# Kernel optimization log

Measured on AMD Instinct MI355X. Metric: run time of the kernel, lower is better.

## Reference

```python
import jax, jax.numpy as jnp
import numpy as np


def setup_inputs() -> dict:
    key = jax.random.key(0)
    ks = jax.random.split(key, 10)
    B, T, E = 4096, 200, 64
    H0, H1, H2 = 80, 40, 1
    D = 4 * E  # concat feature dim = 256
    glorot = lambda k, shp: jax.random.normal(k, shp, jnp.float32) * jnp.sqrt(2.0 / (shp[0] + shp[1]))
    return {
        "queries": jax.random.normal(ks[0], (B, 1, E), jnp.float32),
        "keys": jax.random.normal(ks[1], (B, T, E), jnp.float32),
        "keys_length": jax.random.randint(ks[2], (B, 1), 0, T, jnp.int32),
        "W0": glorot(ks[3], (D, H0)),
        "b0": jnp.zeros((H0,), jnp.float32),
        "W1": glorot(ks[4], (H0, H1)),
        "b1": jnp.zeros((H1,), jnp.float32),
        "W2": glorot(ks[5], (H1, H2)),
        "b2": jnp.zeros((H2,), jnp.float32),
    }


def reference(queries, keys, keys_length, W0, b0, W1, b1, W2, b2):
    B, T, E = keys.shape
    # repeat query along history axis: [B,1,E] -> [B,T,E]
    q = jnp.broadcast_to(queries, (B, T, E))
    # DIN attention input: [B,T,4E]
    att = jnp.concatenate([q, keys, q - keys, q * keys], axis=-1)
    # tiny 3-layer MLP, sigmoid activations (att_activation, no output_activation override)
    h = jax.nn.sigmoid(att @ W0 + b0)
    h = jax.nn.sigmoid(h @ W1 + b1)
    score = jax.nn.sigmoid(h @ W2 + b2)          # [B,T,1]
    out = jnp.transpose(score, (0, 2, 1))         # [B,1,T]
    # sequence mask: [B,1,T]
    key_masks = jnp.arange(T)[None, None, :] < keys_length[:, :, None]
    # weight_normalization=False -> masked positions become 0, no softmax
    out = jnp.where(key_masks, out, jnp.zeros_like(out))
    # weighted sum over history: [B,1,T] @ [B,T,E] -> [B,1,E]
    return jnp.matmul(out, keys)
```

## Files before the change

kernel.cpp:

```cpp
#include <hip/hip_runtime.h>

#define NT 512
#define NWAVE 8
#define PE 136
#define PW1 104
#define PH 104

typedef __attribute__((ext_vector_type(8))) short short8;
typedef __attribute__((ext_vector_type(4))) float f32x4;

#define DPP_ADD(x, ctrl)                                                    \
  ((x) + __uint_as_float(__builtin_amdgcn_mov_dpp(                          \
             __float_as_uint(x), (ctrl), 0xf, 0xf, true)))

__device__ __forceinline__ unsigned short f2b(float f) {
  unsigned int x = __float_as_uint(f);
  return (unsigned short)((x + 0x7fffu + ((x >> 16) & 1u)) >> 16);
}
__device__ __forceinline__ float b2f(unsigned short u) {
  return __uint_as_float(((unsigned int)u) << 16);
}
__device__ __forceinline__ float sigmoidf(float x) {
  return __builtin_amdgcn_rcpf(1.0f + __expf(-x));
}
__device__ __forceinline__ short8 pack8(float4 a, float4 b) {
  short8 r;
  r[0] = (short)f2b(a.x); r[1] = (short)f2b(a.y); r[2] = (short)f2b(a.z); r[3] = (short)f2b(a.w);
  r[4] = (short)f2b(b.x); r[5] = (short)f2b(b.y); r[6] = (short)f2b(b.z); r[7] = (short)f2b(b.w);
  return r;
}
__device__ __forceinline__ short8 pack8qb(float4 a, float4 b, short8 qp) {
  short8 r;
  r[0] = (short)f2b(a.x * b2f((unsigned short)qp[0]));
  r[1] = (short)f2b(a.y * b2f((unsigned short)qp[1]));
  r[2] = (short)f2b(a.z * b2f((unsigned short)qp[2]));
  r[3] = (short)f2b(a.w * b2f((unsigned short)qp[3]));
  r[4] = (short)f2b(b.x * b2f((unsigned short)qp[4]));
  r[5] = (short)f2b(b.y * b2f((unsigned short)qp[5]));
  r[6] = (short)f2b(b.z * b2f((unsigned short)qp[6]));
  r[7] = (short)f2b(b.w * b2f((unsigned short)qp[7]));
  return r;
}

__global__ __launch_bounds__(256, 2) void prep_c(
    const float* __restrict__ q, const float* __restrict__ W0,
    const float* __restrict__ b0, float* __restrict__ C, int B)
{
  __shared__ float Wac[64 * 80];
  __shared__ float qlds[32 * 64];
  const int bbase = blockIdx.x * 32, tid = threadIdx.x;
  for (int idx = tid; idx < 5120; idx += 256) {
    const int e = idx / 80, h = idx - e * 80;
    Wac[idx] = W0[e * 80 + h] + W0[(128 + e) * 80 + h];
  }
  for (int idx = tid; idx < 2048; idx += 256) {
    const int bl = idx >> 6, e = idx & 63;
    const int bg = bbase + bl;
    qlds[idx] = (bg < B) ? q[bg * 64 + e] : 0.0f;
  }
  __syncthreads();
  #pragma unroll
  for (int i = 0; i < 10; ++i) {
    const int idx = tid + i * 256;
    const int bl = idx / 80, h = idx - bl * 80;
    const int bg = bbase + bl;
    if (bg < B) {
      float acc = b0[h];
      #pragma unroll 8
      for (int e = 0; e < 64; ++e) acc += qlds[bl * 64 + e] * Wac[e * 80 + h];
      C[bg * 80 + h] = acc;
    }
  }
}

__global__ __launch_bounds__(NT, 2) void din_attn_main(
    const float* __restrict__ q,
    const float* __restrict__ keys,
    const int* __restrict__ klen,
    const float* __restrict__ W0,
    const float* __restrict__ b0,
    const float* __restrict__ W1,
    const float* __restrict__ b1,
    const float* __restrict__ W2,
    const float* __restrict__ b2,
    float* __restrict__ out,
    const float* __restrict__ Cpre,
    int B)
{
  __shared__ __align__(16) unsigned short WxT[80 * PE];
  __shared__ __align__(16) unsigned short W1T[48 * PW1];
  __shared__ __align__(16) unsigned short h0s[NWAVE][16 * PH];

  const int tid = threadIdx.x;

  for (int idx = tid; idx < 128 * 80; idx += NT) {
    const int e = idx / 80, h = idx - e * 80;
    const float v = (e < 64)
        ? (W0[(64 + e) * 80 + h] - W0[(128 + e) * 80 + h])
        : W0[(128 + e) * 80 + h];
    WxT[h * PE + e] = f2b(v);
  }
  for (int idx = tid; idx < 48 * PW1; idx += NT) {
    const int j = idx / PW1, h = idx - j * PW1;
    W1T[idx] = (j < 40 && h < 80) ? f2b(W1[h * 40 + j]) : (unsigned short)0;
  }
  {
    const int w0i = tid >> 6, ln = tid & 63;
    for (int i = ln; i < 256; i += 64)
      h0s[w0i][(i >> 4) * PH + 80 + (i & 15)] = 0;
  }
  __syncthreads();

  const int wv = __builtin_amdgcn_readfirstlane(tid >> 6);
  const int lane = tid & 63;
  const int lm = lane & 15;
  const int quad = lane >> 4;
  const int b = blockIdx.x * NWAVE + wv;
  if (b >= B) return;

  int L = klen[b];
  L = __builtin_amdgcn_readfirstlane(max(0, min(200, L)));
  unsigned short* h0 = h0s[wv];

  const float4* q4 = (const float4*)(q + (size_t)b * 64);
  const short8 qpk0 = pack8(q4[quad * 2], q4[quad * 2 + 1]);
  const short8 qpk1 = pack8(q4[8 + quad * 2], q4[8 + quad * 2 + 1]);

  float cfv[5];
  if (Cpre != nullptr) {
    #pragma unroll
    for (int nt = 0; nt < 5; ++nt) cfv[nt] = Cpre[b * 80 + nt * 16 + lm];
  } else {
    #pragma unroll
    for (int nt = 0; nt < 5; ++nt) cfv[nt] = b0[nt * 16 + lm];
    for (int e = 0; e < 64; ++e) {
      const float qv = q[(size_t)b * 64 + e];
      #pragma unroll
      for (int nt = 0; nt < 5; ++nt) {
        const int col = nt * 16 + lm;
        cfv[nt] += qv * (W0[e * 80 + col] + W0[(128 + e) * 80 + col]);
      }
    }
  }
  float b1v[3], w2v[3];
  #pragma unroll
  for (int nt = 0; nt < 3; ++nt) {
    const int col = nt * 16 + lm;
    b1v[nt] = (col < 40) ? b1[col] : 0.0f;
    w2v[nt] = (col < 40) ? W2[col] : 0.0f;
  }
  const float b2v = b2[0];
  const short8 z8 = {0, 0, 0, 0, 0, 0, 0, 0};
  const float4 z4 = {0.0f, 0.0f, 0.0f, 0.0f};

  const float* kb = keys + (size_t)b * 12800;
  float4 w4 = {0.0f, 0.0f, 0.0f, 0.0f};
  const int passes = (L + 15) >> 4;

  float4 k0 = z4, k1 = z4, k2 = z4, k3 = z4;
  if (passes > 0 && lm < L) {
    const float4* kp = (const float4*)(kb + (size_t)lm * 64);
    k0 = kp[quad * 2]; k1 = kp[quad * 2 + 1];
    k2 = kp[8 + quad * 2]; k3 = kp[8 + quad * 2 + 1];
  }

  for (int p = 0; p < passes; ++p) {
    const int t0 = p << 4;

    short8 a0 = pack8(k0, k1), a1 = pack8(k2, k3);
    short8 aq0 = pack8qb(k0, k1, qpk0), aq1 = pack8qb(k2, k3, qpk1);
    if (!((t0 + lm) < L)) { a0 = z8; a1 = z8; aq0 = z8; aq1 = z8; }

    float4 kv[4];
    #pragma unroll
    for (int r = 0; r < 4; ++r)
      kv[r] = *(const float4*)(kb + (size_t)min(t0 + 4 * quad + r, 199) * 64 + 4 * lm);

    if (p + 1 < passes) {
      const int t = t0 + 16 + lm;
      if (t < L) {
        const float4* kp = (const float4*)(kb + (size_t)t * 64);
        k0 = kp[quad * 2]; k1 = kp[quad * 2 + 1];
        k2 = kp[8 + quad * 2]; k3 = kp[8 + quad * 2 + 1];
      } else { k0 = z4; k1 = z4; k2 = z4; k3 = z4; }
    }

    __builtin_amdgcn_s_setprio(1);
    #pragma unroll
    for (int nt = 0; nt < 5; ++nt) {
      const int col = nt * 16 + lm;
      const unsigned short* wr = &WxT[col * PE + quad * 8];
      const short8 w0 = *(const short8*)(wr);
      const short8 w1 = *(const short8*)(wr + 32);
      const short8 w2 = *(const short8*)(wr + 64);
      const short8 w3 = *(const short8*)(wr + 96);
      f32x4 acc;
      acc[0] = cfv[nt]; acc[1] = cfv[nt]; acc[2] = cfv[nt]; acc[3] = cfv[nt];
      acc = __builtin_amdgcn_mfma_f32_16x16x32_bf16(a0,  w0, acc, 0, 0, 0);
      acc = __builtin_amdgcn_mfma_f32_16x16x32_bf16(a1,  w1, acc, 0, 0, 0);
      acc = __builtin_amdgcn_mfma_f32_16x16x32_bf16(aq0, w2, acc, 0, 0, 0);
      acc = __builtin_amdgcn_mfma_f32_16x16x32_bf16(aq1, w3, acc, 0, 0, 0);
      #pragma unroll
      for (int r = 0; r < 4; ++r)
        h0[(quad * 4 + r) * PH + col] = f2b(sigmoidf(acc[r]));
    }
    __builtin_amdgcn_s_setprio(0);

    const short8 ha0 = *(const short8*)&h0[lm * PH + quad * 8];
    const short8 ha1 = *(const short8*)&h0[lm * PH + 32 + quad * 8];
    const short8 ha2 = *(const short8*)&h0[lm * PH + 64 + quad * 8];
    float pd[4] = {0.0f, 0.0f, 0.0f, 0.0f};
    __builtin_amdgcn_s_setprio(1);
    #pragma unroll
    for (int nt = 0; nt < 3; ++nt) {
      const int col = nt * 16 + lm;
      const unsigned short* wr = &W1T[col * PW1 + quad * 8];
      const short8 wb0 = *(const short8*)(wr);
      const short8 wb1 = *(const short8*)(wr + 32);
      const short8 wb2 = *(const short8*)(wr + 64);
      f32x4 acc;
      acc[0] = b1v[nt]; acc[1] = b1v[nt]; acc[2] = b1v[nt]; acc[3] = b1v[nt];
      acc = __builtin_amdgcn_mfma_f32_16x16x32_bf16(ha0, wb0, acc, 0, 0, 0);
      acc = __builtin_amdgcn_mfma_f32_16x16x32_bf16(ha1, wb1, acc, 0, 0, 0);
      acc = __builtin_amdgcn_mfma_f32_16x16x32_bf16(ha2, wb2, acc, 0, 0, 0);
      #pragma unroll
      for (int r = 0; r < 4; ++r) pd[r] += sigmoidf(acc[r]) * w2v[nt];
    }
    __builtin_amdgcn_s_setprio(0);

    #pragma unroll
    for (int r = 0; r < 4; ++r) {
      pd[r] = DPP_ADD(pd[r], 0xB1);
      pd[r] = DPP_ADD(pd[r], 0x4E);
      pd[r] = DPP_ADD(pd[r], 0x141);
      pd[r] = DPP_ADD(pd[r], 0x140);
    }
    float sc[4];
    #pragma unroll
    for (int r = 0; r < 4; ++r) {
      const int ta = t0 + 4 * quad + r;
      sc[r] = (ta < L) ? sigmoidf(pd[r] + b2v) : 0.0f;
    }

    #pragma unroll
    for (int r = 0; r < 4; ++r) {
      w4.x += sc[r] * kv[r].x; w4.y += sc[r] * kv[r].y;
      w4.z += sc[r] * kv[r].z; w4.w += sc[r] * kv[r].w;
    }
  }

  w4.x += __shfl_xor(w4.x, 16); w4.y += __shfl_xor(w4.y, 16);
  w4.z += __shfl_xor(w4.z, 16); w4.w += __shfl_xor(w4.w, 16);
  w4.x += __shfl_xor(w4.x, 32); w4.y += __shfl_xor(w4.y, 32);
  w4.z += __shfl_xor(w4.z, 32); w4.w += __shfl_xor(w4.w, 32);
  if (lane < 16)
    *(float4*)(out + (size_t)b * 64 + 4 * lm) = w4;
}

extern "C" void kernel_launch(void* const* d_in, const int* in_sizes, int n_in,
                              void* d_out, int out_size, void* d_ws, size_t ws_size,
                              hipStream_t stream) {
  const int B = in_sizes[2];
  const float* Cpre = nullptr;
  if (ws_size >= (size_t)B * 80 * sizeof(float)) {
    float* C = (float*)d_ws;
    prep_c<<<(B + 31) / 32, 256, 0, stream>>>(
        (const float*)d_in[0], (const float*)d_in[3], (const float*)d_in[4], C, B);
    Cpre = C;
  }
  din_attn_main<<<(B + NWAVE - 1) / NWAVE, NT, 0, stream>>>(
      (const float*)d_in[0], (const float*)d_in[1], (const int*)d_in[2],
      (const float*)d_in[3], (const float*)d_in[4], (const float*)d_in[5],
      (const float*)d_in[6], (const float*)d_in[7], (const float*)d_in[8],
      (float*)d_out, Cpre, B);
}
```

Measured before the change: 320.3 us.

## Split each batch row across two waves and keep MLP weights in registers

Each batch row is now handled by two waves that take alternating 16-step tiles of the history, and their partial weighted sums are combined with atomicAdd into a zero-initialised output. This doubles the number of waves to raise occupancy and latency hiding. The W0 and W1 MFMA operand fragments are loaded once into registers rather than re-read from LDS on every pass. LDS is aliased so the per-wave h0 scratch reuses the weight staging area, and the key rows for the weighted sum are now loaded late instead of prefetched. The costs are an extra memset, atomics on the output, higher register pressure (launch bounds relaxed to one block per CU), and a non-deterministic order of the final summation.

```diff
diff --git a/kernel.cpp b/kernel.cpp
--- a/kernel.cpp
+++ b/kernel.cpp
@@ -3,8 +3,9 @@
 #define NT 512
 #define NWAVE 8
 #define PE 136
-#define PW1 104
-#define PH 104
+#define PW1 88
+#define PH 88
+#define SMEM_BYTES 30208
 
 typedef __attribute__((ext_vector_type(8))) short short8;
 typedef __attribute__((ext_vector_type(4))) float f32x4;
@@ -73,7 +74,7 @@
   }
 }
 
-__global__ __launch_bounds__(NT, 2) void din_attn_main(
+__global__ __launch_bounds__(NT, 1) void din_attn_main(
     const float* __restrict__ q,
     const float* __restrict__ keys,
     const int* __restrict__ klen,
@@ -87,9 +88,9 @@
     const float* __restrict__ Cpre,
     int B)
 {
-  __shared__ __align__(16) unsigned short WxT[80 * PE];
-  __shared__ __align__(16) unsigned short W1T[48 * PW1];
-  __shared__ __align__(16) unsigned short h0s[NWAVE][16 * PH];
+  __shared__ __align__(16) unsigned char smem[SMEM_BYTES];
+  unsigned short* WxT = (unsigned short*)smem;
+  unsigned short* W1T = (unsigned short*)(smem + 21760);
 
   const int tid = threadIdx.x;
 
@@ -104,23 +105,42 @@
     const int j = idx / PW1, h = idx - j * PW1;
     W1T[idx] = (j < 40 && h < 80) ? f2b(W1[h * 40 + j]) : (unsigned short)0;
   }
-  {
-    const int w0i = tid >> 6, ln = tid & 63;
-    for (int i = ln; i < 256; i += 64)
-      h0s[w0i][(i >> 4) * PH + 80 + (i & 15)] = 0;
-  }
   __syncthreads();
 
   const int wv = __builtin_amdgcn_readfirstlane(tid >> 6);
   const int lane = tid & 63;
   const int lm = lane & 15;
   const int quad = lane >> 4;
-  const int b = blockIdx.x * NWAVE + wv;
+  const short8 z8 = {0, 0, 0, 0, 0, 0, 0, 0};
+  const float4 z4 = {0.0f, 0.0f, 0.0f, 0.0f};
+
+  short8 wx[5][4];
+  #pragma unroll
+  for (int nt = 0; nt < 5; ++nt) {
+    const unsigned short* wr = &WxT[(nt * 16 + lm) * PE + quad * 8];
+    #pragma unroll
+    for (int s = 0; s < 4; ++s) wx[nt][s] = *(const short8*)(wr + 32 * s);
+  }
+  short8 w1f[3][3];
+  #pragma unroll
+  for (int nt = 0; nt < 3; ++nt) {
+    const unsigned short* wr = &W1T[(nt * 16 + lm) * PW1 + quad * 8];
+    w1f[nt][0] = *(const short8*)(wr);
+    w1f[nt][1] = *(const short8*)(wr + 32);
+    w1f[nt][2] = (quad < 2) ? *(const short8*)(wr + 64) : z8;
+  }
+  __syncthreads();
+
+  unsigned short* h0 = (unsigned short*)smem + wv * (16 * PH);
+
+  const int gw = blockIdx.x * NWAVE + wv;
+  const int b = gw >> 1;
+  const int half = gw & 1;
   if (b >= B) return;
 
   int L = klen[b];
   L = __builtin_amdgcn_readfirstlane(max(0, min(200, L)));
-  unsigned short* h0 = h0s[wv];
+  const int nu = (L + 15) >> 4;
 
   const float4* q4 = (const float4*)(q + (size_t)b * 64);
   const short8 qpk0 = pack8(q4[quad * 2], q4[quad * 2 + 1]);
@@ -150,34 +170,29 @@
     w2v[nt] = (col < 40) ? W2[col] : 0.0f;
   }
   const float b2v = b2[0];
-  const short8 z8 = {0, 0, 0, 0, 0, 0, 0, 0};
-  const float4 z4 = {0.0f, 0.0f, 0.0f, 0.0f};
 
   const float* kb = keys + (size_t)b * 12800;
   float4 w4 = {0.0f, 0.0f, 0.0f, 0.0f};
-  const int passes = (L + 15) >> 4;
 
   float4 k0 = z4, k1 = z4, k2 = z4, k3 = z4;
-  if (passes > 0 && lm < L) {
-    const float4* kp = (const float4*)(kb + (size_t)lm * 64);
-    k0 = kp[quad * 2]; k1 = kp[quad * 2 + 1];
-    k2 = kp[8 + quad * 2]; k3 = kp[8 + quad * 2 + 1];
-  }
-
-  for (int p = 0; p < passes; ++p) {
+  if (half < nu) {
+    const int t = (half << 4) + lm;
+    if (t < L) {
+      const float4* kp = (const float4*)(kb + (size_t)t * 64);
+      k0 = kp[quad * 2]; k1 = kp[quad * 2 + 1];
+      k2 = kp[8 + quad * 2]; k3 = kp[8 + quad * 2 + 1];
+    }
+  }
+
+  for (int p = half; p < nu; p += 2) {
     const int t0 = p << 4;
 
     short8 a0 = pack8(k0, k1), a1 = pack8(k2, k3);
     short8 aq0 = pack8qb(k0, k1, qpk0), aq1 = pack8qb(k2, k3, qpk1);
     if (!((t0 + lm) < L)) { a0 = z8; a1 = z8; aq0 = z8; aq1 = z8; }
 
-    float4 kv[4];
-    #pragma unroll
-    for (int r = 0; r < 4; ++r)
-      kv[r] = *(const float4*)(kb + (size_t)min(t0 + 4 * quad + r, 199) * 64 + 4 * lm);
-
-    if (p + 1 < passes) {
-      const int t = t0 + 16 + lm;
+    if (p + 2 < nu) {
+      const int t = ((p + 2) << 4) + lm;
       if (t < L) {
         const float4* kp = (const float4*)(kb + (size_t)t * 64);
         k0 = kp[quad * 2]; k1 = kp[quad * 2 + 1];
@@ -189,17 +204,12 @@
     #pragma unroll
     for (int nt = 0; nt < 5; ++nt) {
       const int col = nt * 16 + lm;
-      const unsigned short* wr = &WxT[col * PE + quad * 8];
-      const short8 w0 = *(const short8*)(wr);
-      const short8 w1 = *(const short8*)(wr + 32);
-      const short8 w2 = *(const short8*)(wr + 64);
-      const short8 w3 = *(const short8*)(wr + 96);
       f32x4 acc;
       acc[0] = cfv[nt]; acc[1] = cfv[nt]; acc[2] = cfv[nt]; acc[3] = cfv[nt];
-      acc = __builtin_amdgcn_mfma_f32_16x16x32_bf16(a0,  w0, acc, 0, 0, 0);
-      acc = __builtin_amdgcn_mfma_f32_16x16x32_bf16(a1,  w1, acc, 0, 0, 0);
-      acc = __builtin_amdgcn_mfma_f32_16x16x32_bf16(aq0, w2, acc, 0, 0, 0);
-      acc = __builtin_amdgcn_mfma_f32_16x16x32_bf16(aq1, w3, acc, 0, 0, 0);
+      acc = __builtin_amdgcn_mfma_f32_16x16x32_bf16(a0,  wx[nt][0], acc, 0, 0, 0);
+      acc = __builtin_amdgcn_mfma_f32_16x16x32_bf16(a1,  wx[nt][1], acc, 0, 0, 0);
+      acc = __builtin_amdgcn_mfma_f32_16x16x32_bf16(aq0, wx[nt][2], acc, 0, 0, 0);
+      acc = __builtin_amdgcn_mfma_f32_16x16x32_bf16(aq1, wx[nt][3], acc, 0, 0, 0);
       #pragma unroll
       for (int r = 0; r < 4; ++r)
         h0[(quad * 4 + r) * PH + col] = f2b(sigmoidf(acc[r]));
@@ -208,21 +218,16 @@
 
     const short8 ha0 = *(const short8*)&h0[lm * PH + quad * 8];
     const short8 ha1 = *(const short8*)&h0[lm * PH + 32 + quad * 8];
-    const short8 ha2 = *(const short8*)&h0[lm * PH + 64 + quad * 8];
+    const short8 ha2 = (quad < 2) ? *(const short8*)&h0[lm * PH + 64 + quad * 8] : z8;
     float pd[4] = {0.0f, 0.0f, 0.0f, 0.0f};
     __builtin_amdgcn_s_setprio(1);
     #pragma unroll
     for (int nt = 0; nt < 3; ++nt) {
-      const int col = nt * 16 + lm;
-      const unsigned short* wr = &W1T[col * PW1 + quad * 8];
-      const short8 wb0 = *(const short8*)(wr);
-      const short8 wb1 = *(const short8*)(wr + 32);
-      const short8 wb2 = *(const short8*)(wr + 64);
       f32x4 acc;
       acc[0] = b1v[nt]; acc[1] = b1v[nt]; acc[2] = b1v[nt]; acc[3] = b1v[nt];
-      acc = __builtin_amdgcn_mfma_f32_16x16x32_bf16(ha0, wb0, acc, 0, 0, 0);
-      acc = __builtin_amdgcn_mfma_f32_16x16x32_bf16(ha1, wb1, acc, 0, 0, 0);
-      acc = __builtin_amdgcn_mfma_f32_16x16x32_bf16(ha2, wb2, acc, 0, 0, 0);
+      acc = __builtin_amdgcn_mfma_f32_16x16x32_bf16(ha0, w1f[nt][0], acc, 0, 0, 0);
+      acc = __builtin_amdgcn_mfma_f32_16x16x32_bf16(ha1, w1f[nt][1], acc, 0, 0, 0);
+      acc = __builtin_amdgcn_mfma_f32_16x16x32_bf16(ha2, w1f[nt][2], acc, 0, 0, 0);
       #pragma unroll
       for (int r = 0; r < 4; ++r) pd[r] += sigmoidf(acc[r]) * w2v[nt];
     }
@@ -244,8 +249,9 @@
 
     #pragma unroll
     for (int r = 0; r < 4; ++r) {
-      w4.x += sc[r] * kv[r].x; w4.y += sc[r] * kv[r].y;
-      w4.z += sc[r] * kv[r].z; w4.w += sc[r] * kv[r].w;
+      const float4 kv = *(const float4*)(kb + (size_t)min(t0 + 4 * quad + r, 199) * 64 + 4 * lm);
+      w4.x += sc[r] * kv.x; w4.y += sc[r] * kv.y;
+      w4.z += sc[r] * kv.z; w4.w += sc[r] * kv.w;
     }
   }
 
@@ -253,8 +259,11 @@
   w4.z += __shfl_xor(w4.z, 16); w4.w += __shfl_xor(w4.w, 16);
   w4.x += __shfl_xor(w4.x, 32); w4.y += __shfl_xor(w4.y, 32);
   w4.z += __shfl_xor(w4.z, 32); w4.w += __shfl_xor(w4.w, 32);
-  if (lane < 16)
-    *(float4*)(out + (size_t)b * 64 + 4 * lm) = w4;
+  if (lane < 16) {
+    float* op = out + (size_t)b * 64 + 4 * lm;
+    atomicAdd(op + 0, w4.x); atomicAdd(op + 1, w4.y);
+    atomicAdd(op + 2, w4.z); atomicAdd(op + 3, w4.w);
+  }
 }
 
 extern "C" void kernel_launch(void* const* d_in, const int* in_sizes, int n_in,
@@ -262,13 +271,15 @@
                               hipStream_t stream) {
   const int B = in_sizes[2];
   const float* Cpre = nullptr;
+  hipMemsetAsync(d_out, 0, (size_t)out_size, stream);
   if (ws_size >= (size_t)B * 80 * sizeof(float)) {
     float* C = (float*)d_ws;
     prep_c<<<(B + 31) / 32, 256, 0, stream>>>(
         (const float*)d_in[0], (const float*)d_in[3], (const float*)d_in[4], C, B);
     Cpre = C;
   }
-  din_attn_main<<<(B + NWAVE - 1) / NWAVE, NT, 0, stream>>>(
+  const int nwaves = 2 * B;
+  din_attn_main<<<(nwaves + NWAVE - 1) / NWAVE, NT, 0, stream>>>(
       (const float*)d_in[0], (const float*)d_in[1], (const int*)d_in[2],
       (const float*)d_in[3], (const float*)d_in[4], (const float*)d_in[5],
       (const float*)d_in[6], (const float*)d_in[7], (const float*)d_in[8],
```

Result: slower. 342.1 us (+6.8%).
